# Optimization experiments

Measured on AMD Instinct MI355X. Metric: run time of the kernel, lower is better.

## Reference

```python
import jax, jax.numpy as jnp
import numpy as np

N, E = 50000, 800000
IN_CH, HID, MSG_HID, L = 128, 256, 128, 10
EPS = 1e-5


def _xavier(key, shape):
    fan_in, fan_out = shape[-2], shape[-1]
    lim = np.sqrt(6.0 / (fan_in + fan_out))
    return jax.random.uniform(key, shape, jnp.float32, -lim, lim)


def setup_inputs() -> dict:
    key = jax.random.key(0)
    ks = jax.random.split(key, 10)
    x = jax.random.normal(ks[0], (N, IN_CH), jnp.float32)
    edge_index = jax.random.randint(ks[1], (2, E), 0, N, jnp.int32)
    Win = _xavier(ks[2], (IN_CH, HID))
    bin_ = jnp.zeros((HID,), jnp.float32)
    # per-layer stacked params [L, ...]
    W1 = _xavier(ks[3], (L, HID, MSG_HID))
    b1 = jnp.zeros((L, MSG_HID), jnp.float32)
    W2 = _xavier(ks[4], (L, MSG_HID, HID))
    b2 = jnp.zeros((L, HID), jnp.float32)
    U1 = _xavier(ks[5], (L, HID, HID))
    c1 = jnp.zeros((L, HID), jnp.float32)
    U2 = _xavier(ks[6], (L, HID, HID))
    c2 = jnp.zeros((L, HID), jnp.float32)
    ln_g = jnp.ones((L, HID), jnp.float32)
    ln_b = jnp.zeros((L, HID), jnp.float32)
    beta = 0.01 * jax.random.normal(ks[7], (L + 1,), jnp.float32)
    return {"x": x, "edge_index": edge_index, "Win": Win, "bin_": bin_,
            "W1": W1, "b1": b1, "W2": W2, "b2": b2,
            "U1": U1, "c1": c1, "U2": U2, "c2": c2,
            "ln_g": ln_g, "ln_b": ln_b, "beta": beta}


def reference(x, edge_index, Win, bin_, W1, b1, W2, b2, U1, c1, U2, c2, ln_g, ln_b, beta):
    n = x.shape[0]
    self_loop = jnp.arange(n, dtype=edge_index.dtype)
    src = jnp.concatenate([edge_index[0], self_loop])  # x_j (source)
    dst = jnp.concatenate([edge_index[1], self_loop])  # aggregate at target i
    counts = jax.ops.segment_sum(jnp.ones_like(dst, dtype=x.dtype), dst, num_segments=n)
    counts = counts[:, None]  # >=1 thanks to self loops

    z0 = x @ Win + bin_  # input_lin, use_activation=False

    def layer(z, p):
        w1, bb1, w2, bb2, u1, cc1, u2, cc2, g, b_ = p
        msg = jax.nn.relu(z[src] @ w1 + bb1) @ w2 + bb2       # [E+N, HID]
        m = jax.ops.segment_sum(msg, dst, num_segments=n) / counts
        h = z + m
        out = jax.nn.relu(h @ u1 + cc1) @ u2 + cc2
        mu = out.mean(-1, keepdims=True)
        var = out.var(-1, keepdims=True)
        out = (out - mu) * jax.lax.rsqrt(var + EPS) * g + b_
        return out, out

    _, zs = jax.lax.scan(layer, z0, (W1, b1, W2, b2, U1, c1, U2, c2, ln_g, ln_b))
    zs_all = jnp.concatenate([z0[None], zs], axis=0)  # [L+1, N, HID]
    betas = jax.nn.softmax(beta)
    return jnp.einsum('l,lnh->nh', betas, zs_all)
```

## Files before the change

### kernel.cpp

```cpp
#include <hip/hip_runtime.h>
#include <stdint.h>

typedef __attribute__((ext_vector_type(4))) float f32x4;
typedef __attribute__((ext_vector_type(8))) short bf16x8;

#define HIDC 256
#define MSGC 128
#define NLAYER 10

__device__ __forceinline__ ushort f2bf(float f) {
  union { float f; uint32_t u; } a; a.f = f;
  uint32_t u = a.u;
  return (ushort)((u + 0x7fffu + ((u >> 16) & 1u)) >> 16);
}
__device__ __forceinline__ float bf2f(ushort h) {
  union { float f; uint32_t u; } a; a.u = ((uint32_t)h) << 16;
  return a.f;
}

__device__ __forceinline__ void gll16(const void* g, void* l) {
  __builtin_amdgcn_global_load_lds(
      (const __attribute__((address_space(1))) void*)g,
      (__attribute__((address_space(3))) void*)l, 16, 0, 0);
}

__global__ __launch_bounds__(256, 4) void gemm_w1_64(
    const ushort* __restrict__ A, const ushort* __restrict__ B,
    const float* __restrict__ bias, ushort* __restrict__ C, int M) {
  __shared__ ushort lA[64 * 64];
  __shared__ ushort lB[128 * 64];
  const int tid = threadIdx.x;
  const int m0 = blockIdx.x * 64;
  const int lane = tid & 63;
  const int w = tid >> 6;
  const int wm = (w >> 1) * 32;
  const int wn = (w & 1) * 64;
  const int rr = tid >> 3;
  const int cc = tid & 7;
  const int ccs = cc ^ (rr & 7);
  const bool full = (m0 + 64 <= M);
  f32x4 acc[2][4] = {};

#pragma unroll
  for (int s = 0; s < 4; ++s) {
    const int k0 = s * 64;
    if (full) {
#pragma unroll
      for (int p = 0; p < 2; ++p) {
        const int row = p * 32 + rr;
        gll16(A + (size_t)(m0 + row) * 256 + k0 + ccs * 8,
              lA + (size_t)(p * 32 + w * 8) * 64);
      }
    } else {
#pragma unroll
      for (int p = 0; p < 2; ++p) {
        const int row = p * 32 + rr;
        const int gm = m0 + row;
        bf16x8 av = {0, 0, 0, 0, 0, 0, 0, 0};
        if (gm < M) av = *(const bf16x8*)(A + (size_t)gm * 256 + k0 + cc * 8);
        const uint32_t off = (uint32_t)((row * 128 + cc * 16) ^ ((row & 7) << 4));
        *(bf16x8*)((char*)lA + off) = av;
      }
    }
#pragma unroll
    for (int p = 0; p < 4; ++p) {
      const int row = p * 32 + rr;
      gll16(B + (size_t)row * 256 + k0 + ccs * 8,
            lB + (size_t)(p * 32 + w * 8) * 64);
    }
    __syncthreads();
#pragma unroll
    for (int kk = 0; kk < 2; ++kk) {
      bf16x8 ah[2];
#pragma unroll
      for (int i = 0; i < 2; ++i) {
        const int arow = wm + i * 16 + (lane & 15);
        const uint32_t ao =
            (uint32_t)((arow * 128 + kk * 64 + ((lane >> 4) * 16)) ^ ((arow & 7) << 4));
        ah[i] = *(const bf16x8*)((const char*)lA + ao);
      }
#pragma unroll
      for (int j = 0; j < 4; ++j) {
        const int brow = wn + j * 16 + (lane & 15);
        const uint32_t bo =
            (uint32_t)((brow * 128 + kk * 64 + ((lane >> 4) * 16)) ^ ((brow & 7) << 4));
        const bf16x8 bv = *(const bf16x8*)((const char*)lB + bo);
#pragma unroll
        for (int i = 0; i < 2; ++i)
          acc[i][j] = __builtin_amdgcn_mfma_f32_16x16x32_bf16(ah[i], bv, acc[i][j], 0, 0, 0);
      }
    }
    __syncthreads();
  }
  float bi[4];
#pragma unroll
  for (int j = 0; j < 4; ++j) bi[j] = bias[wn + j * 16 + (lane & 15)];
#pragma unroll
  for (int i = 0; i < 2; ++i) {
    const int gm0 = m0 + wm + i * 16 + ((lane >> 4) << 2);
#pragma unroll
    for (int r = 0; r < 4; ++r) {
      const int gm = gm0 + r;
      if (gm < M) {
        const size_t base = (size_t)gm * 128 + wn + (lane & 15);
#pragma unroll
        for (int j = 0; j < 4; ++j)
          C[base + j * 16] = f2bf(fmaxf(acc[i][j][r] + bi[j], 0.f));
      }
    }
  }
}

template <int RELU, int ADDZ, int LN>
__global__ __launch_bounds__(256, 3) void gemm_big64(
    const ushort* __restrict__ A, const ushort* __restrict__ B,
    const float* __restrict__ bias, const ushort* __restrict__ Z,
    ushort* __restrict__ C, const float* __restrict__ g,
    const float* __restrict__ b_, int M, int K) {
  __shared__ ushort lA[64 * 64];
  __shared__ ushort lB[256 * 64];
  __shared__ float sstat[2][4][64];
  const int tid = threadIdx.x;
  const int m0 = blockIdx.x * 64;
  const int lane = tid & 63;
  const int w = tid >> 6;
  const int wn = w * 64;
  const int rr = tid >> 3;
  const int cc = tid & 7;
  const int ccs = cc ^ (rr & 7);
  const bool full = (m0 + 64 <= M);
  f32x4 acc[4][4] = {};

  const int nsteps = K >> 6;
  for (int s = 0; s < nsteps; ++s) {
    const int k0 = s * 64;
    if (full) {
#pragma unroll
      for (int p = 0; p < 2; ++p) {
        const int row = p * 32 + rr;
        gll16(A + (size_t)(m0 + row) * K + k0 + ccs * 8,
              lA + (size_t)(p * 32 + w * 8) * 64);
      }
    } else {
#pragma unroll
      for (int p = 0; p < 2; ++p) {
        const int row = p * 32 + rr;
        const int gm = m0 + row;
        bf16x8 av = {0, 0, 0, 0, 0, 0, 0, 0};
        if (gm < M) av = *(const bf16x8*)(A + (size_t)gm * K + k0 + cc * 8);
        const uint32_t off = (uint32_t)((row * 128 + cc * 16) ^ ((row & 7) << 4));
        *(bf16x8*)((char*)lA + off) = av;
      }
    }
#pragma unroll
    for (int p = 0; p < 8; ++p) {
      const int row = p * 32 + rr;
      gll16(B + (size_t)row * K + k0 + ccs * 8,
            lB + (size_t)(p * 32 + w * 8) * 64);
    }
    __syncthreads();
#pragma unroll
    for (int kk = 0; kk < 2; ++kk) {
      bf16x8 ah[4];
#pragma unroll
      for (int i = 0; i < 4; ++i) {
        const int arow = i * 16 + (lane & 15);
        const uint32_t ao =
            (uint32_t)((arow * 128 + kk * 64 + ((lane >> 4) * 16)) ^ ((arow & 7) << 4));
        ah[i] = *(const bf16x8*)((const char*)lA + ao);
      }
#pragma unroll
      for (int j = 0; j < 4; ++j) {
        const int brow = wn + j * 16 + (lane & 15);
        const uint32_t bo =
            (uint32_t)((brow * 128 + kk * 64 + ((lane >> 4) * 16)) ^ ((brow & 7) << 4));
        const bf16x8 bv = *(const bf16x8*)((const char*)lB + bo);
#pragma unroll
        for (int i = 0; i < 4; ++i)
          acc[i][j] = __builtin_amdgcn_mfma_f32_16x16x32_bf16(ah[i], bv, acc[i][j], 0, 0, 0);
      }
    }
    __syncthreads();
  }

  float bi[4];
#pragma unroll
  for (int j = 0; j < 4; ++j) bi[j] = bias[wn + j * 16 + (lane & 15)];

  if (LN) {
    float gv[4], bv[4];
#pragma unroll
    for (int j = 0; j < 4; ++j) {
      gv[j] = g[wn + j * 16 + (lane & 15)];
      bv[j] = b_[wn + j * 16 + (lane & 15)];
    }
#pragma unroll
    for (int i = 0; i < 4; ++i) {
#pragma unroll
      for (int r = 0; r < 4; ++r) {
        float s1 = 0.f, s2 = 0.f;
#pragma unroll
        for (int j = 0; j < 4; ++j) {
          float v = acc[i][j][r] + bi[j];
          acc[i][j][r] = v;
          s1 += v;
          s2 += v * v;
        }
#pragma unroll
        for (int d = 1; d < 16; d <<= 1) {
          s1 += __shfl_xor(s1, d);
          s2 += __shfl_xor(s2, d);
        }
        if ((lane & 15) == 0) {
          const int rl = i * 16 + ((lane >> 4) << 2) + r;
          sstat[0][w][rl] = s1;
          sstat[1][w][rl] = s2;
        }
      }
    }
    __syncthreads();
#pragma unroll
    for (int i = 0; i < 4; ++i) {
#pragma unroll
      for (int r = 0; r < 4; ++r) {
        const int rl = i * 16 + ((lane >> 4) << 2) + r;
        const float s1 = sstat[0][0][rl] + sstat[0][1][rl] + sstat[0][2][rl] + sstat[0][3][rl];
        const float s2 = sstat[1][0][rl] + sstat[1][1][rl] + sstat[1][2][rl] + sstat[1][3][rl];
        const float mu = s1 * (1.f / 256.f);
        const float var = s2 * (1.f / 256.f) - mu * mu;
        const float rs = rsqrtf(var + 1e-5f);
        const int gm = m0 + rl;
        if (gm < M) {
          const size_t base = (size_t)gm * 256 + wn + (lane & 15);
#pragma unroll
          for (int j = 0; j < 4; ++j)
            C[base + j * 16] = f2bf((acc[i][j][r] - mu) * rs * gv[j] + bv[j]);
        }
      }
    }
  } else {
#pragma unroll
    for (int i = 0; i < 4; ++i) {
      const int gm0 = m0 + i * 16 + ((lane >> 4) << 2);
#pragma unroll
      for (int r = 0; r < 4; ++r) {
        const int gm = gm0 + r;
        if (gm < M) {
          const size_t base = (size_t)gm * 256 + wn + (lane & 15);
#pragma unroll
          for (int j = 0; j < 4; ++j) {
            float v = acc[i][j][r] + bi[j];
            if (ADDZ) v += bf2f(Z[base + j * 16]);
            if (RELU) v = fmaxf(v, 0.f);
            C[base + j * 16] = f2bf(v);
          }
        }
      }
    }
  }
}

template <int WRITE>
__global__ __launch_bounds__(256) void fold_kernel(
    const ushort* __restrict__ zbase, size_t ZS, const float* __restrict__ betas,
    int l0, int P, float* __restrict__ outp, int total8) {
  const int i = blockIdx.x * 256 + threadIdx.x;
  if (i >= total8) return;
  float a[8] = {};
  for (int k = 0; k < P; ++k) {
    const float bl = betas[l0 + k];
    const uint4 u = ((const uint4*)(zbase + k * ZS))[i];
    const uint32_t ww[4] = {u.x, u.y, u.z, u.w};
#pragma unroll
    for (int q = 0; q < 4; ++q) {
      union { uint32_t u; float f; } lo, hi;
      lo.u = ww[q] << 16;
      hi.u = ww[q] & 0xffff0000u;
      a[2 * q] += bl * lo.f;
      a[2 * q + 1] += bl * hi.f;
    }
  }
  f32x4 o0 = {a[0], a[1], a[2], a[3]};
  f32x4 o1 = {a[4], a[5], a[6], a[7]};
  if (WRITE) {
    ((f32x4*)outp)[(size_t)i * 2] = o0;
    ((f32x4*)outp)[(size_t)i * 2 + 1] = o1;
  } else {
    f32x4 p0 = ((f32x4*)outp)[(size_t)i * 2];
    f32x4 p1 = ((f32x4*)outp)[(size_t)i * 2 + 1];
    ((f32x4*)outp)[(size_t)i * 2] = p0 + o0;
    ((f32x4*)outp)[(size_t)i * 2 + 1] = p1 + o1;
  }
}

__global__ void count_kernel(const int* __restrict__ dstv, int* __restrict__ deg, int E) {
  int i = blockIdx.x * 256 + threadIdx.x;
  if (i < E) atomicAdd(&deg[dstv[i]], 1);
}

__global__ void scanA_kernel(const int* __restrict__ deg, int* __restrict__ excl,
                             int* __restrict__ bsum, int n) {
  __shared__ int sm[256];
  const int i = blockIdx.x * 256 + threadIdx.x;
  const int v = (i < n) ? deg[i] : 0;
  sm[threadIdx.x] = v;
  __syncthreads();
  for (int off = 1; off < 256; off <<= 1) {
    int t = (threadIdx.x >= off) ? sm[threadIdx.x - off] : 0;
    __syncthreads();
    sm[threadIdx.x] += t;
    __syncthreads();
  }
  if (i < n) excl[i] = sm[threadIdx.x] - v;
  if (threadIdx.x == 255) bsum[blockIdx.x] = sm[255];
}

__global__ void scanB_kernel(const int* __restrict__ bsum, int* __restrict__ boff, int nb) {
  __shared__ int sm[256];
  const int v = (threadIdx.x < nb) ? bsum[threadIdx.x] : 0;
  sm[threadIdx.x] = v;
  __syncthreads();
  for (int off = 1; off < 256; off <<= 1) {
    int t = (threadIdx.x >= off) ? sm[threadIdx.x - off] : 0;
    __syncthreads();
    sm[threadIdx.x] += t;
    __syncthreads();
  }
  if (threadIdx.x < nb) boff[threadIdx.x] = sm[threadIdx.x] - v;
}

__global__ void scanC_kernel(const int* __restrict__ deg, const int* __restrict__ excl,
                             const int* __restrict__ boff, int* __restrict__ rowptr,
                             int* __restrict__ fillptr, float* __restrict__ invc,
                             int n, int E) {
  const int i = blockIdx.x * 256 + threadIdx.x;
  if (i < n) {
    const int r = excl[i] + boff[blockIdx.x];
    rowptr[i] = r;
    fillptr[i] = r;
    invc[i] = 1.0f / (float)(deg[i] + 1);
  }
  if (i == 0) rowptr[n] = E;
}

__global__ void fill_kernel(const int* __restrict__ srcv, const int* __restrict__ dstv,
                            int* __restrict__ fillptr, int* __restrict__ colv, int E) {
  int i = blockIdx.x * 256 + threadIdx.x;
  if (i < E) {
    int p = atomicAdd(&fillptr[dstv[i]], 1);
    colv[p] = srcv[i];
  }
}

__global__ __launch_bounds__(256) void agg128_kernel(
    const ushort* __restrict__ T, const int* __restrict__ rowptr,
    const int* __restrict__ colv, const float* __restrict__ invc,
    ushort* __restrict__ sout, int n) {
  const int node = blockIdx.x * 16 + (threadIdx.x >> 4);
  if (node >= n) return;
  const int q = threadIdx.x & 15;
  const uint4* Tv = (const uint4*)T;
  float a[8] = {}, b[8] = {}, c[8] = {}, d[8] = {};
  auto addu = [](float* acc, uint4 u) {
    const uint32_t ww[4] = {u.x, u.y, u.z, u.w};
#pragma unroll
    for (int k = 0; k < 4; ++k) {
      union { uint32_t u; float f; } lo, hi;
      lo.u = ww[k] << 16;
      hi.u = ww[k] & 0xffff0000u;
      acc[2 * k] += lo.f;
      acc[2 * k + 1] += hi.f;
    }
  };
  addu(a, Tv[(size_t)node * 16 + q]);
  const int s = rowptr[node];
  const int e = rowptr[node + 1];
  int i = s;
  for (; i + 3 < e; i += 4) {
    const uint4 u0 = Tv[(size_t)colv[i] * 16 + q];
    const uint4 u1 = Tv[(size_t)colv[i + 1] * 16 + q];
    const uint4 u2 = Tv[(size_t)colv[i + 2] * 16 + q];
    const uint4 u3 = Tv[(size_t)colv[i + 3] * 16 + q];
    addu(a, u0);
    addu(b, u1);
    addu(c, u2);
    addu(d, u3);
  }
  for (; i < e; ++i) addu(a, Tv[(size_t)colv[i] * 16 + q]);
  const float ic = invc[node];
  uint4 o;
  uint32_t* ow = (uint32_t*)&o;
#pragma unroll
  for (int k = 0; k < 4; ++k) {
    const float r0 = (a[2 * k] + b[2 * k] + c[2 * k] + d[2 * k]) * ic;
    const float r1 = (a[2 * k + 1] + b[2 * k + 1] + c[2 * k + 1] + d[2 * k + 1]) * ic;
    ow[k] = (uint32_t)f2bf(r0) | ((uint32_t)f2bf(r1) << 16);
  }
  ((uint4*)sout)[(size_t)node * 16 + q] = o;
}

__global__ void beta_kernel(const float* __restrict__ beta, float* __restrict__ betas) {
  if (threadIdx.x == 0) {
    float mx = beta[0];
    for (int i = 1; i < NLAYER + 1; ++i) mx = fmaxf(mx, beta[i]);
    float e[NLAYER + 1];
    float s = 0.f;
    for (int i = 0; i < NLAYER + 1; ++i) {
      e[i] = expf(beta[i] - mx);
      s += e[i];
    }
    const float inv = 1.f / s;
    for (int i = 0; i < NLAYER + 1; ++i) betas[i] = e[i] * inv;
  }
}

__global__ void wconv_kernel(const float* __restrict__ W, ushort* __restrict__ Wt,
                             int K, int Nn) {
  const size_t matoff = (size_t)blockIdx.z * K * Nn;
  const int o = blockIdx.x * 256 + threadIdx.x;
  if (o >= K * Nn) return;
  const int nn = o / K;
  const int kk = o - nn * K;
  Wt[matoff + o] = f2bf(W[matoff + (size_t)kk * Nn + nn]);
}

__global__ void wconvU_kernel(const float* __restrict__ U1, const float* __restrict__ U2,
                              ushort* __restrict__ U1T, ushort* __restrict__ U2T) {
  const int li = blockIdx.z;
  const float* W = (li < NLAYER) ? U1 : U2;
  ushort* Wt = (li < NLAYER) ? U1T : U2T;
  const size_t matoff = (size_t)(li % NLAYER) * 256 * 256;
  const int o = blockIdx.x * 256 + threadIdx.x;
  const int nn = o >> 8;
  const int kk = o & 255;
  Wt[matoff + o] = f2bf(W[matoff + (size_t)kk * 256 + nn]);
}

__global__ void xcast_kernel(const float* __restrict__ x, ushort* __restrict__ xb, int n8) {
  const int i = blockIdx.x * 256 + threadIdx.x;
  if (i >= n8) return;
  const f32x4 v0 = ((const f32x4*)x)[(size_t)i * 2];
  const f32x4 v1 = ((const f32x4*)x)[(size_t)i * 2 + 1];
  bf16x8 o;
#pragma unroll
  for (int q = 0; q < 4; ++q) {
    o[q] = (short)f2bf(v0[q]);
    o[q + 4] = (short)f2bf(v1[q]);
  }
  *(bf16x8*)(xb + (size_t)i * 8) = o;
}

__global__ __launch_bounds__(512, 4) void gemm_win(
    const ushort* __restrict__ A, const ushort* __restrict__ B,
    const float* __restrict__ bias, ushort* __restrict__ C, int M) {
  __shared__ ushort lA[128 * 64];
  __shared__ ushort lB[256 * 64];
  const int tid = threadIdx.x;
  const int m0 = blockIdx.x * 128;
  const int lane = tid & 63;
  const int w = tid >> 6;
  const int wm = (w >> 2) * 64;
  const int wn = (w & 3) * 64;
  const int rr = tid >> 3;
  const int cc = tid & 7;
  const int ccs = cc ^ (rr & 7);
  const bool full = (m0 + 128 <= M);
  f32x4 acc[4][4] = {};
  const int K = 128;

#pragma unroll
  for (int s = 0; s < 2; ++s) {
    const int k0 = s * 64;
    if (full) {
#pragma unroll
      for (int p = 0; p < 2; ++p) {
        const int row = p * 64 + rr;
        gll16(A + (size_t)(m0 + row) * K + k0 + ccs * 8,
              lA + (size_t)(p * 64 + w * 8) * 64);
      }
    } else {
#pragma unroll
      for (int p = 0; p < 2; ++p) {
        const int row = p * 64 + rr;
        const int gm = m0 + row;
        bf16x8 av = {0, 0, 0, 0, 0, 0, 0, 0};
        if (gm < M) av = *(const bf16x8*)(A + (size_t)gm * K + k0 + cc * 8);
        const uint32_t off = (uint32_t)((row * 128 + cc * 16) ^ ((row & 7) << 4));
        *(bf16x8*)((char*)lA + off) = av;
      }
    }
#pragma unroll
    for (int p = 0; p < 4; ++p) {
      const int row = p * 64 + rr;
      gll16(B + (size_t)row * K + k0 + ccs * 8,
            lB + (size_t)(p * 64 + w * 8) * 64);
    }
    __syncthreads();
#pragma unroll
    for (int kk = 0; kk < 2; ++kk) {
      bf16x8 ah[4];
#pragma unroll
      for (int i = 0; i < 4; ++i) {
        const int arow = wm + i * 16 + (lane & 15);
        const uint32_t ao =
            (uint32_t)((arow * 128 + kk * 64 + ((lane >> 4) * 16)) ^ ((arow & 7) << 4));
        ah[i] = *(const bf16x8*)((const char*)lA + ao);
      }
#pragma unroll
      for (int j = 0; j < 4; ++j) {
        const int brow = wn + j * 16 + (lane & 15);
        const uint32_t bo =
            (uint32_t)((brow * 128 + kk * 64 + ((lane >> 4) * 16)) ^ ((brow & 7) << 4));
        const bf16x8 bv = *(const bf16x8*)((const char*)lB + bo);
#pragma unroll
        for (int i = 0; i < 4; ++i)
          acc[i][j] = __builtin_amdgcn_mfma_f32_16x16x32_bf16(ah[i], bv, acc[i][j], 0, 0, 0);
      }
    }
    __syncthreads();
  }
  float bi[4];
#pragma unroll
  for (int j = 0; j < 4; ++j) bi[j] = bias[wn + j * 16 + (lane & 15)];
#pragma unroll
  for (int i = 0; i < 4; ++i) {
    const int gm0 = m0 + wm + i * 16 + ((lane >> 4) << 2);
#pragma unroll
    for (int r = 0; r < 4; ++r) {
      const int gm = gm0 + r;
      if (gm < M) {
        const size_t base = (size_t)gm * 256 + wn + (lane & 15);
#pragma unroll
        for (int j = 0; j < 4; ++j)
          C[base + j * 16] = f2bf(acc[i][j][r] + bi[j]);
      }
    }
  }
}

extern "C" void kernel_launch(void* const* d_in, const int* in_sizes, int n_in,
                              void* d_out, int out_size, void* d_ws, size_t ws_size,
                              hipStream_t stream) {
  const float* x = (const float*)d_in[0];
  const int* eidx = (const int*)d_in[1];
  const float* Win = (const float*)d_in[2];
  const float* bin_ = (const float*)d_in[3];
  const float* W1 = (const float*)d_in[4];
  const float* b1 = (const float*)d_in[5];
  const float* W2 = (const float*)d_in[6];
  const float* b2 = (const float*)d_in[7];
  const float* U1 = (const float*)d_in[8];
  const float* c1 = (const float*)d_in[9];
  const float* U2 = (const float*)d_in[10];
  const float* c2 = (const float*)d_in[11];
  const float* ln_g = (const float*)d_in[12];
  const float* ln_b = (const float*)d_in[13];
  const float* beta = (const float*)d_in[14];
  float* outp = (float*)d_out;

  const int Nn = in_sizes[0] / 128;
  const int E = in_sizes[1] / 2;
  const int* srcv = eidx;
  const int* dstv = eidx + E;

  char* p = (char*)d_ws;
  auto alloc = [&](size_t bytes) {
    char* r = p;
    p += (bytes + 255) & ~(size_t)255;
    return r;
  };
  ushort* hbuf = (ushort*)alloc((size_t)Nn * HIDC * 2);
  ushort* TSO = (ushort*)alloc((size_t)Nn * HIDC * 2);
  ushort* xbf = (ushort*)alloc((size_t)Nn * 128 * 2);
  ushort* WinT = (ushort*)alloc(128 * 256 * 2);
  ushort* W1T = (ushort*)alloc((size_t)NLAYER * 256 * 128 * 2);
  ushort* W2T = (ushort*)alloc((size_t)NLAYER * 128 * 256 * 2);
  ushort* U1T = (ushort*)alloc((size_t)NLAYER * 256 * 256 * 2);
  ushort* U2T = (ushort*)alloc((size_t)NLAYER * 256 * 256 * 2);
  int* deg = (int*)alloc((size_t)Nn * 4);
  int* rowptr = (int*)alloc((size_t)(Nn + 1) * 4);
  int* fillptr = (int*)alloc((size_t)Nn * 4);
  float* invc = (float*)alloc((size_t)Nn * 4);
  int* colv = (int*)alloc((size_t)E * 4);
  int* excl = (int*)alloc((size_t)Nn * 4);
  int* bsum = (int*)alloc(256 * 4);
  int* boff = (int*)alloc(256 * 4);
  float* betas = (float*)alloc(64);

  const size_t ZS = (size_t)Nn * HIDC;
  const size_t slotB = ZS * 2;
  const size_t used = (size_t)(p - (char*)d_ws);
  int G = 2;
  if (ws_size > used + 4096) {
    size_t fit = (ws_size - used - 4096) / (slotB + 256);
    G = (int)(fit < 2 ? 2 : (fit > NLAYER + 1 ? NLAYER + 1 : fit));
  }
  ushort* zbase = (ushort*)alloc((size_t)G * slotB);

  ushort* T128 = TSO;
  ushort* s128 = TSO + (size_t)Nn * MSGC;
  ushort* Obuf = TSO;

  const int nscan = (Nn + 255) / 256;
  const int mb128 = (Nn + 127) / 128;
  const int mb64 = (Nn + 63) / 64;
  const int nagg = (Nn + 15) / 16;
  const int total8 = (Nn * HIDC) / 8;

  hipMemsetAsync(deg, 0, (size_t)Nn * 4, stream);
  count_kernel<<<(E + 255) / 256, 256, 0, stream>>>(dstv, deg, E);
  scanA_kernel<<<nscan, 256, 0, stream>>>(deg, excl, bsum, Nn);
  scanB_kernel<<<1, 256, 0, stream>>>(bsum, boff, nscan);
  scanC_kernel<<<nscan, 256, 0, stream>>>(deg, excl, boff, rowptr, fillptr, invc, Nn, E);
  fill_kernel<<<(E + 255) / 256, 256, 0, stream>>>(srcv, dstv, fillptr, colv, E);
  beta_kernel<<<1, 64, 0, stream>>>(beta, betas);
  xcast_kernel<<<(Nn * 16 + 255) / 256, 256, 0, stream>>>(x, xbf, Nn * 16);
  wconv_kernel<<<dim3(128, 1, 1), 256, 0, stream>>>(Win, WinT, 128, 256);
  wconv_kernel<<<dim3(128, 1, NLAYER), 256, 0, stream>>>(W1, W1T, 256, 128);
  wconv_kernel<<<dim3(128, 1, NLAYER), 256, 0, stream>>>(W2, W2T, 128, 256);
  wconvU_kernel<<<dim3(256, 1, 2 * NLAYER), 256, 0, stream>>>(U1, U2, U1T, U2T);

  int pend = 0, l0 = 0;
  bool first = true;
  auto flush = [&]() {
    if (pend > 0) {
      if (first)
        fold_kernel<1><<<(total8 + 255) / 256, 256, 0, stream>>>(zbase, ZS, betas, l0,
                                                                 pend, outp, total8);
      else
        fold_kernel<0><<<(total8 + 255) / 256, 256, 0, stream>>>(zbase, ZS, betas, l0,
                                                                 pend, outp, total8);
      first = false;
      l0 += pend;
      pend = 0;
    }
  };

  ushort* zcur = zbase;
  gemm_win<<<mb128, 512, 0, stream>>>(xbf, WinT, bin_, zcur, Nn);
  pend = 1;

  for (int l = 0; l < NLAYER; ++l) {
    gemm_w1_64<<<mb64, 256, 0, stream>>>(zcur, W1T + (size_t)l * 256 * 128,
                                         b1 + l * 128, T128, Nn);
    agg128_kernel<<<nagg, 256, 0, stream>>>(T128, rowptr, colv, invc, s128, Nn);
    gemm_big64<0, 1, 0><<<mb64, 256, 0, stream>>>(s128, W2T + (size_t)l * 128 * 256,
                                                  b2 + l * 256, zcur, hbuf, nullptr,
                                                  nullptr, Nn, 128);
    gemm_big64<1, 0, 0><<<mb64, 256, 0, stream>>>(hbuf, U1T + (size_t)l * 256 * 256,
                                                  c1 + l * 256, nullptr, Obuf, nullptr,
                                                  nullptr, Nn, 256);
    if (pend == G) flush();
    ushort* znext = zbase + (size_t)pend * ZS;
    gemm_big64<0, 0, 1><<<mb64, 256, 0, stream>>>(Obuf, U2T + (size_t)l * 256 * 256,
                                                  c2 + l * 256, nullptr, znext,
                                                  ln_g + l * 256, ln_b + l * 256, Nn, 256);
    zcur = znext;
    pend++;
  }
  flush();
}
```

Measured before the change: 1.261 ms.

## Double-buffer big GEMM LDS tiles, drop fill atomics, tile weight transposes

The 64-row GEMM now stages K in 32-wide slices into two LDS buffers. The next slice loads while the current one feeds MFMA, with one barrier per step instead of two. The CSR build records each edge's atomic slot during counting, so the fill pass no longer needs a second atomic. Weight conversion uses a shared-memory 32x32 tiled transpose for coalesced reads and writes. The risks are more K iterations with half the work each, and an extra E-sized offset buffer.

```diff
diff --git a/kernel.cpp b/kernel.cpp
--- a/kernel.cpp
+++ b/kernel.cpp
@@ -117,71 +117,66 @@
     const float* __restrict__ bias, const ushort* __restrict__ Z,
     ushort* __restrict__ C, const float* __restrict__ g,
     const float* __restrict__ b_, int M, int K) {
-  __shared__ ushort lA[64 * 64];
-  __shared__ ushort lB[256 * 64];
+  __shared__ ushort lA[2][64 * 32];
+  __shared__ ushort lB[2][256 * 32];
   __shared__ float sstat[2][4][64];
   const int tid = threadIdx.x;
   const int m0 = blockIdx.x * 64;
   const int lane = tid & 63;
   const int w = tid >> 6;
   const int wn = w * 64;
-  const int rr = tid >> 3;
-  const int cc = tid & 7;
-  const int ccs = cc ^ (rr & 7);
+  const int srow = tid >> 2;
+  const int scc = tid & 3;
   const bool full = (m0 + 64 <= M);
   f32x4 acc[4][4] = {};
-
-  const int nsteps = K >> 6;
+  const int nsteps = K >> 5;
+
+  auto stage = [&](int s, int buf) {
+    const int k0 = s * 32;
+    if (full) {
+      const int ccs = scc ^ ((srow >> 1) & 3);
+      gll16(A + (size_t)(m0 + srow) * K + k0 + ccs * 8, &lA[buf][(w * 16) * 32]);
+    } else {
+      const int gm = m0 + srow;
+      bf16x8 av = {0, 0, 0, 0, 0, 0, 0, 0};
+      if (gm < M) av = *(const bf16x8*)(A + (size_t)gm * K + k0 + scc * 8);
+      const uint32_t off = (uint32_t)((srow * 64 + scc * 16) ^ ((srow & 6) << 3));
+      *(bf16x8*)((char*)lA[buf] + off) = av;
+    }
+#pragma unroll
+    for (int p = 0; p < 4; ++p) {
+      const int row = p * 64 + srow;
+      const int ccs = scc ^ ((row >> 1) & 3);
+      gll16(B + (size_t)row * K + k0 + ccs * 8, &lB[buf][(p * 64 + w * 16) * 32]);
+    }
+  };
+
+  int cur = 0;
+  stage(0, 0);
   for (int s = 0; s < nsteps; ++s) {
-    const int k0 = s * 64;
-    if (full) {
-#pragma unroll
-      for (int p = 0; p < 2; ++p) {
-        const int row = p * 32 + rr;
-        gll16(A + (size_t)(m0 + row) * K + k0 + ccs * 8,
-              lA + (size_t)(p * 32 + w * 8) * 64);
-      }
-    } else {
-#pragma unroll
-      for (int p = 0; p < 2; ++p) {
-        const int row = p * 32 + rr;
-        const int gm = m0 + row;
-        bf16x8 av = {0, 0, 0, 0, 0, 0, 0, 0};
-        if (gm < M) av = *(const bf16x8*)(A + (size_t)gm * K + k0 + cc * 8);
-        const uint32_t off = (uint32_t)((row * 128 + cc * 16) ^ ((row & 7) << 4));
-        *(bf16x8*)((char*)lA + off) = av;
-      }
-    }
-#pragma unroll
-    for (int p = 0; p < 8; ++p) {
-      const int row = p * 32 + rr;
-      gll16(B + (size_t)row * K + k0 + ccs * 8,
-            lB + (size_t)(p * 32 + w * 8) * 64);
-    }
-    __syncthreads();
-#pragma unroll
-    for (int kk = 0; kk < 2; ++kk) {
-      bf16x8 ah[4];
-#pragma unroll
-      for (int i = 0; i < 4; ++i) {
-        const int arow = i * 16 + (lane & 15);
-        const uint32_t ao =
-            (uint32_t)((arow * 128 + kk * 64 + ((lane >> 4) * 16)) ^ ((arow & 7) << 4));
-        ah[i] = *(const bf16x8*)((const char*)lA + ao);
-      }
-#pragma unroll
-      for (int j = 0; j < 4; ++j) {
-        const int brow = wn + j * 16 + (lane & 15);
-        const uint32_t bo =
-            (uint32_t)((brow * 128 + kk * 64 + ((lane >> 4) * 16)) ^ ((brow & 7) << 4));
-        const bf16x8 bv = *(const bf16x8*)((const char*)lB + bo);
-#pragma unroll
-        for (int i = 0; i < 4; ++i)
-          acc[i][j] = __builtin_amdgcn_mfma_f32_16x16x32_bf16(ah[i], bv, acc[i][j], 0, 0, 0);
-      }
-    }
-    __syncthreads();
-  }
+    __syncthreads();
+    if (s + 1 < nsteps) stage(s + 1, cur ^ 1);
+    bf16x8 ah[4];
+#pragma unroll
+    for (int i = 0; i < 4; ++i) {
+      const int arow = i * 16 + (lane & 15);
+      const uint32_t ao =
+          (uint32_t)((arow * 64 + ((lane >> 4) * 16)) ^ ((arow & 6) << 3));
+      ah[i] = *(const bf16x8*)((const char*)lA[cur] + ao);
+    }
+#pragma unroll
+    for (int j = 0; j < 4; ++j) {
+      const int brow = wn + j * 16 + (lane & 15);
+      const uint32_t bo =
+          (uint32_t)((brow * 64 + ((lane >> 4) * 16)) ^ ((brow & 6) << 3));
+      const bf16x8 bv = *(const bf16x8*)((const char*)lB[cur] + bo);
+#pragma unroll
+      for (int i = 0; i < 4; ++i)
+        acc[i][j] = __builtin_amdgcn_mfma_f32_16x16x32_bf16(ah[i], bv, acc[i][j], 0, 0, 0);
+    }
+    cur ^= 1;
+  }
+  __syncthreads();
 
   float bi[4];
 #pragma unroll
@@ -293,9 +288,10 @@
   }
 }
 
-__global__ void count_kernel(const int* __restrict__ dstv, int* __restrict__ deg, int E) {
+__global__ void count_kernel(const int* __restrict__ dstv, int* __restrict__ deg,
+                             int* __restrict__ eoff, int E) {
   int i = blockIdx.x * 256 + threadIdx.x;
-  if (i < E) atomicAdd(&deg[dstv[i]], 1);
+  if (i < E) eoff[i] = atomicAdd(&deg[dstv[i]], 1);
 }
 
 __global__ void scanA_kernel(const int* __restrict__ deg, int* __restrict__ excl,
@@ -331,25 +327,20 @@
 
 __global__ void scanC_kernel(const int* __restrict__ deg, const int* __restrict__ excl,
                              const int* __restrict__ boff, int* __restrict__ rowptr,
-                             int* __restrict__ fillptr, float* __restrict__ invc,
-                             int n, int E) {
+                             float* __restrict__ invc, int n, int E) {
   const int i = blockIdx.x * 256 + threadIdx.x;
   if (i < n) {
-    const int r = excl[i] + boff[blockIdx.x];
-    rowptr[i] = r;
-    fillptr[i] = r;
+    rowptr[i] = excl[i] + boff[blockIdx.x];
     invc[i] = 1.0f / (float)(deg[i] + 1);
   }
   if (i == 0) rowptr[n] = E;
 }
 
 __global__ void fill_kernel(const int* __restrict__ srcv, const int* __restrict__ dstv,
-                            int* __restrict__ fillptr, int* __restrict__ colv, int E) {
+                            const int* __restrict__ rowptr, const int* __restrict__ eoff,
+                            int* __restrict__ colv, int E) {
   int i = blockIdx.x * 256 + threadIdx.x;
-  if (i < E) {
-    int p = atomicAdd(&fillptr[dstv[i]], 1);
-    colv[p] = srcv[i];
-  }
+  if (i < E) colv[rowptr[dstv[i]] + eoff[i]] = srcv[i];
 }
 
 __global__ __launch_bounds__(256) void agg128_kernel(
@@ -414,26 +405,21 @@
   }
 }
 
-__global__ void wconv_kernel(const float* __restrict__ W, ushort* __restrict__ Wt,
-                             int K, int Nn) {
-  const size_t matoff = (size_t)blockIdx.z * K * Nn;
-  const int o = blockIdx.x * 256 + threadIdx.x;
-  if (o >= K * Nn) return;
-  const int nn = o / K;
-  const int kk = o - nn * K;
-  Wt[matoff + o] = f2bf(W[matoff + (size_t)kk * Nn + nn]);
-}
-
-__global__ void wconvU_kernel(const float* __restrict__ U1, const float* __restrict__ U2,
-                              ushort* __restrict__ U1T, ushort* __restrict__ U2T) {
-  const int li = blockIdx.z;
-  const float* W = (li < NLAYER) ? U1 : U2;
-  ushort* Wt = (li < NLAYER) ? U1T : U2T;
-  const size_t matoff = (size_t)(li % NLAYER) * 256 * 256;
-  const int o = blockIdx.x * 256 + threadIdx.x;
-  const int nn = o >> 8;
-  const int kk = o & 255;
-  Wt[matoff + o] = f2bf(W[matoff + (size_t)kk * 256 + nn]);
+__global__ void wconv_t(const float* __restrict__ W, ushort* __restrict__ Wt,
+                        int K, int Nn) {
+  __shared__ float t[32][33];
+  const size_t mat = (size_t)blockIdx.z * K * Nn;
+  const int kk0 = blockIdx.x * 32;
+  const int nn0 = blockIdx.y * 32;
+  const int tx = threadIdx.x & 31;
+  const int ty = threadIdx.x >> 5;
+#pragma unroll
+  for (int i = 0; i < 4; ++i)
+    t[ty * 4 + i][tx] = W[mat + (size_t)(kk0 + ty * 4 + i) * Nn + nn0 + tx];
+  __syncthreads();
+#pragma unroll
+  for (int i = 0; i < 4; ++i)
+    Wt[mat + (size_t)(nn0 + ty * 4 + i) * K + kk0 + tx] = f2bf(t[tx][ty * 4 + i]);
 }
 
 __global__ void xcast_kernel(const float* __restrict__ x, ushort* __restrict__ xb, int n8) {
@@ -579,9 +565,9 @@
   ushort* U2T = (ushort*)alloc((size_t)NLAYER * 256 * 256 * 2);
   int* deg = (int*)alloc((size_t)Nn * 4);
   int* rowptr = (int*)alloc((size_t)(Nn + 1) * 4);
-  int* fillptr = (int*)alloc((size_t)Nn * 4);
   float* invc = (float*)alloc((size_t)Nn * 4);
   int* colv = (int*)alloc((size_t)E * 4);
+  int* eoff = (int*)alloc((size_t)E * 4);
   int* excl = (int*)alloc((size_t)Nn * 4);
   int* bsum = (int*)alloc(256 * 4);
   int* boff = (int*)alloc(256 * 4);
@@ -608,17 +594,18 @@
   const int total8 = (Nn * HIDC) / 8;
 
   hipMemsetAsync(deg, 0, (size_t)Nn * 4, stream);
-  count_kernel<<<(E + 255) / 256, 256, 0, stream>>>(dstv, deg, E);
+  count_kernel<<<(E + 255) / 256, 256, 0, stream>>>(dstv, deg, eoff, E);
   scanA_kernel<<<nscan, 256, 0, stream>>>(deg, excl, bsum, Nn);
   scanB_kernel<<<1, 256, 0, stream>>>(bsum, boff, nscan);
-  scanC_kernel<<<nscan, 256, 0, stream>>>(deg, excl, boff, rowptr, fillptr, invc, Nn, E);
-  fill_kernel<<<(E + 255) / 256, 256, 0, stream>>>(srcv, dstv, fillptr, colv, E);
+  scanC_kernel<<<nscan, 256, 0, stream>>>(deg, excl, boff, rowptr, invc, Nn, E);
+  fill_kernel<<<(E + 255) / 256, 256, 0, stream>>>(srcv, dstv, rowptr, eoff, colv, E);
   beta_kernel<<<1, 64, 0, stream>>>(beta, betas);
   xcast_kernel<<<(Nn * 16 + 255) / 256, 256, 0, stream>>>(x, xbf, Nn * 16);
-  wconv_kernel<<<dim3(128, 1, 1), 256, 0, stream>>>(Win, WinT, 128, 256);
-  wconv_kernel<<<dim3(128, 1, NLAYER), 256, 0, stream>>>(W1, W1T, 256, 128);
-  wconv_kernel<<<dim3(128, 1, NLAYER), 256, 0, stream>>>(W2, W2T, 128, 256);
-  wconvU_kernel<<<dim3(256, 1, 2 * NLAYER), 256, 0, stream>>>(U1, U2, U1T, U2T);
+  wconv_t<<<dim3(4, 8, 1), 256, 0, stream>>>(Win, WinT, 128, 256);
+  wconv_t<<<dim3(8, 4, NLAYER), 256, 0, stream>>>(W1, W1T, 256, 128);
+  wconv_t<<<dim3(4, 8, NLAYER), 256, 0, stream>>>(W2, W2T, 128, 256);
+  wconv_t<<<dim3(8, 8, NLAYER), 256, 0, stream>>>(U1, U1T, 256, 256);
+  wconv_t<<<dim3(8, 8, NLAYER), 256, 0, stream>>>(U2, U2T, 256, 256);
 
   int pend = 0, l0 = 0;
   bool first = true;
```

Result: no change. 1.273 ms (+0.9%).
